# Performance work log

Hardware: AMD Instinct MI355X
Metric: run time of the kernel (lower is better)

Reference implementation:

```python
import jax, jax.numpy as jnp
import numpy as np

B, SQ, SK = 2, 2048, 2048
D, H = 1024, 16
HD = D // H              # head_dim = 64
R = 128                  # rel_pos_max_distance
P = 2 * R + 1            # num_pos_ids = 257
RADIUS = 256             # local_attention_radius


def setup_inputs() -> dict:
    key = jax.random.key(0)
    ks = jax.random.split(key, 8)
    s = 0.02
    return {
        "Q": jax.random.normal(ks[0], (B, SQ, D), dtype=jnp.float32),
        "K": jax.random.normal(ks[1], (B, SK, D), dtype=jnp.float32),
        "V": jax.random.normal(ks[2], (B, SK, D), dtype=jnp.float32),
        "Wq": jax.random.normal(ks[3], (D, D), dtype=jnp.float32) * s,
        "Wk": jax.random.normal(ks[4], (D, D), dtype=jnp.float32) * s,
        "Wv": jax.random.normal(ks[5], (D, D), dtype=jnp.float32) * s,
        "Wo": jax.random.normal(ks[6], (D, D), dtype=jnp.float32) * s,
        "E": jax.random.normal(ks[7], (P, D), dtype=jnp.float32) * s,  # rel_embeds
    }


def _split_heads(x, W):
    # bias-free projection then split: B x S x D -> B x H x S x HD
    y = x @ W.T
    b, s, _ = y.shape
    return y.reshape(b, s, H, HD).transpose(0, 2, 1, 3)


def reference(Q, K, V, Wq, Wk, Wv, Wo, E):
    q = _split_heads(Q, Wq)  # B,H,Sq,HD
    k = _split_heads(K, Wk)  # B,H,Sk,HD
    v = _split_heads(V, Wv)  # B,H,Sk,HD

    # rel_embeds reshape matches torch: E[p] viewed as (head_dim, num_heads)
    rel = E.reshape(P, HD, H).transpose(2, 0, 1)           # H,P,HD
    Q_rel = jnp.einsum("bhqd,hpd->bhqp", q, rel)           # B,H,Sq,P

    # slided relative position ids: clip(j - i, -R, R) + R
    i = jnp.arange(SQ)[:, None]
    j = jnp.arange(SK)[None, :]
    rel_ids = jnp.clip(j - i, -R, R) + R                   # Sq,Sk
    rel_shift = jnp.take_along_axis(
        Q_rel, jnp.broadcast_to(rel_ids, (B, H, SQ, SK)), axis=3
    )                                                       # B,H,Sq,Sk

    energy = (jnp.einsum("bhqd,bhkd->bhqk", q, k) + rel_shift) / jnp.sqrt(
        jnp.float32(HD)
    )

    # local attention mask: True = masked (outside window of radius RADIUS)
    mask = jnp.abs(j - i) > RADIUS                          # Sq,Sk
    mask = mask & ~jnp.all(mask, axis=-1, keepdims=True)    # never mask full rows
    energy = jnp.where(mask[None, None], -jnp.inf, energy)

    attn = jax.nn.softmax(energy, axis=-1)                  # B,H,Sq,Sk
    out = jnp.einsum("bhqk,bhkd->bhqd", attn, v)            # B,H,Sq,HD
    # torch: view(B,H,Sq,HD).permute(0,2,3,1).flatten(2,3) -> B,Sq,(HD*H)
    out = out.transpose(0, 2, 3, 1).reshape(B, SQ, D)
    return out @ Wo.T
```

## Files before the change

### kernel.cpp

```cpp
#include <hip/hip_runtime.h>
#include <hip/hip_bf16.h>

#define BATCH 2
#define SQn 2048
#define SKn 2048
#define DMODEL 1024
#define NH 16
#define HD 64
#define NPOS 257
#define RWIN 128
#define RADIUS 256

typedef __attribute__((ext_vector_type(8))) short bf16x8;
typedef __attribute__((ext_vector_type(4))) float f32x4;

static __device__ __forceinline__ unsigned short f2bf(float f) {
    union { float f; unsigned u; } v; v.f = f;
    unsigned r = (v.u + 0x7FFFu + ((v.u >> 16) & 1u)) >> 16;
    return (unsigned short)r;
}
static __device__ __forceinline__ float bf2f(unsigned short b) {
    union { unsigned u; float f; } v; v.u = ((unsigned)b) << 16;
    return v.f;
}

static __device__ __forceinline__ void gl_lds16(const unsigned short* g, unsigned short* l) {
    __builtin_amdgcn_global_load_lds(
        (const __attribute__((address_space(1))) unsigned*)g,
        (__attribute__((address_space(3))) unsigned*)l, 16, 0, 0);
}

#define SWZ(row) (((row) ^ ((row) >> 2)) & 3)

__global__ __launch_bounds__(256) void convert_kernel(
    const float* __restrict__ Q, const float* __restrict__ K, const float* __restrict__ V,
    const float* __restrict__ Wq, const float* __restrict__ Wk, const float* __restrict__ Wv,
    const float* __restrict__ Wo,
    unsigned short* __restrict__ xb,
    unsigned short* __restrict__ wb,
    unsigned short* __restrict__ woh)
{
    int i = blockIdx.x * 256 + threadIdx.x;
    if (i < 3145728) {
        int which = i >> 20;
        int off = i & 1048575;
        const float* src = which == 0 ? Q : (which == 1 ? K : V);
        unsigned short* dst = xb + (size_t)which * 4194304;
        float4 v4 = ((const float4*)src)[off];
        ushort4 o4;
        o4.x = f2bf(v4.x); o4.y = f2bf(v4.y); o4.z = f2bf(v4.z); o4.w = f2bf(v4.w);
        ((ushort4*)dst)[off] = o4;
    } else {
        int i2 = i - 3145728;
        int which = i2 >> 18;
        int off = i2 & 262143;
        if (which < 3) {
            const float* src = which == 0 ? Wq : (which == 1 ? Wk : Wv);
            unsigned short* dst = wb + (size_t)which * 1048576;
            float4 v4 = ((const float4*)src)[off];
            ushort4 o4;
            o4.x = f2bf(v4.x); o4.y = f2bf(v4.y); o4.z = f2bf(v4.z); o4.w = f2bf(v4.w);
            ((ushort4*)dst)[off] = o4;
        } else {
            float4 v4 = ((const float4*)Wo)[off];
            int e0 = off * 4;
            int n  = e0 >> 10;
            int c0 = e0 & 1023;
            int d  = c0 >> 4;
            int h0 = c0 & 15;
            woh[((size_t)(h0 + 0) * 1024 + n) * 64 + d] = f2bf(v4.x);
            woh[((size_t)(h0 + 1) * 1024 + n) * 64 + d] = f2bf(v4.y);
            woh[((size_t)(h0 + 2) * 1024 + n) * 64 + d] = f2bf(v4.z);
            woh[((size_t)(h0 + 3) * 1024 + n) * 64 + d] = f2bf(v4.w);
        }
    }
}

__global__ __launch_bounds__(256) void mfma_gemm(
    const unsigned short* __restrict__ Xall,
    const unsigned short* __restrict__ Wall,
    unsigned short* __restrict__ Yall)
{
    __shared__ unsigned short sA[128 * 32];
    __shared__ unsigned short sB[128 * 32];
    __shared__ unsigned short sT[64 * 136];

    const int tid  = threadIdx.x;
    const int wv   = tid >> 6;
    const int lane = tid & 63;
    const int quad = lane >> 4;
    const int l15  = lane & 15;
    const int z    = blockIdx.z;
    const int m0   = blockIdx.x * 128;
    const int n0   = blockIdx.y * 128;
    const int wr   = (wv >> 1) * 64;
    const int wc   = (wv & 1) * 64;

    const unsigned short* X = Xall + (size_t)z * (4096 * 1024);
    const unsigned short* W = Wall + (size_t)z * (1024 * 1024);

    int aoff[4], boff[4];
#pragma unroll
    for (int t = 0; t < 4; ++t) {
        int row = wr + t * 16 + l15;
        aoff[t] = row * 32 + ((quad ^ SWZ(row)) * 8);
        int col = wc + t * 16 + l15;
        boff[t] = col * 32 + ((quad ^ SWZ(col)) * 8);
    }

    int srow[2], scg[2], sf[2];
#pragma unroll
    for (int r = 0; r < 2; ++r) {
        int f = r * 256 + tid;
        sf[r] = f;
        srow[r] = f >> 2;
        scg[r] = (f & 3) ^ SWZ(srow[r]);
    }

    f32x4 acc[4][4];
#pragma unroll
    for (int i = 0; i < 4; ++i)
#pragma unroll
        for (int j = 0; j < 4; ++j)
            acc[i][j] = (f32x4){0.f, 0.f, 0.f, 0.f};

    for (int k0 = 0; k0 < 1024; k0 += 32) {
        __syncthreads();
#pragma unroll
        for (int r = 0; r < 2; ++r) {
            gl_lds16(X + (size_t)(m0 + srow[r]) * 1024 + k0 + scg[r] * 8, &sA[sf[r] * 8]);
            gl_lds16(W + (size_t)(n0 + srow[r]) * 1024 + k0 + scg[r] * 8, &sB[sf[r] * 8]);
        }
        __syncthreads();

        bf16x8 af[4], bfr[4];
#pragma unroll
        for (int t = 0; t < 4; ++t) af[t]  = *(const bf16x8*)&sA[aoff[t]];
#pragma unroll
        for (int t = 0; t < 4; ++t) bfr[t] = *(const bf16x8*)&sB[boff[t]];
#pragma unroll
        for (int i = 0; i < 4; ++i)
#pragma unroll
            for (int j = 0; j < 4; ++j)
                acc[i][j] = __builtin_amdgcn_mfma_f32_16x16x32_bf16(af[i], bfr[j], acc[i][j], 0, 0, 0);
    }

    unsigned short* Y = Yall + (size_t)z * (4096 * 1024);
    const int b_ = m0 >> 11;
    const int s0 = m0 & (SQn - 1);

    if (z < 2) {
#pragma unroll
        for (int i = 0; i < 4; ++i) {
            int mbase = s0 + wr + i * 16 + quad * 4;
#pragma unroll
            for (int j = 0; j < 4; ++j) {
                int col = n0 + wc + j * 16 + l15;
                int h = col >> 6, dd = col & 63;
                unsigned short* yb = Y + (((size_t)(b_ * NH + h) * SQn) << 6) + dd;
#pragma unroll
                for (int r = 0; r < 4; ++r)
                    yb[(size_t)(mbase + r) << 6] = f2bf(acc[i][j][r]);
            }
        }
    } else {
#pragma unroll
        for (int hh = 0; hh < 2; ++hh) {
            __syncthreads();
            if ((wv & 1) == hh) {
#pragma unroll
                for (int i = 0; i < 4; ++i) {
                    int mloc = wr + i * 16 + quad * 4;
#pragma unroll
                    for (int j = 0; j < 4; ++j) {
                        ushort4 pk;
                        pk.x = f2bf(acc[i][j][0]);
                        pk.y = f2bf(acc[i][j][1]);
                        pk.z = f2bf(acc[i][j][2]);
                        pk.w = f2bf(acc[i][j][3]);
                        *(ushort4*)&sT[(j * 16 + l15) * 136 + mloc] = pk;
                    }
                }
            }
            __syncthreads();
            int h = (n0 >> 6) + hh;
            unsigned short* yb = Y + ((size_t)(b_ * NH + h) * HD) * SKn + s0;
#pragma unroll
            for (int it = 0; it < 4; ++it) {
                int u = it * 256 + tid;
                int dd = u >> 4, mc = u & 15;
                uint4 val = *(const uint4*)&sT[dd * 136 + mc * 8];
                *(uint4*)(yb + (size_t)dd * SKn + mc * 8) = val;
            }
        }
    }
}

__global__ __launch_bounds__(256) void gemm_out(
    const unsigned short* __restrict__ aoh,
    const unsigned short* __restrict__ woh,
    float* __restrict__ Y)
{
    __shared__ unsigned short sA[64 * 32];
    __shared__ unsigned short sB[128 * 32];

    const int tid  = threadIdx.x;
    const int wv   = tid >> 6;
    const int lane = tid & 63;
    const int quad = lane >> 4;
    const int l15  = lane & 15;
    const int m0   = blockIdx.x * 64;
    const int n0   = blockIdx.y * 128;
    const int wr   = (wv >> 1) * 32;
    const int wc   = (wv & 1) * 64;
    const int b_   = m0 >> 11;
    const int s0   = m0 & (SQn - 1);

    int aoff[2], boff[4];
#pragma unroll
    for (int i = 0; i < 2; ++i) {
        int row = wr + i * 16 + l15;
        aoff[i] = row * 32 + ((quad ^ SWZ(row)) * 8);
    }
#pragma unroll
    for (int j = 0; j < 4; ++j) {
        int col = wc + j * 16 + l15;
        boff[j] = col * 32 + ((quad ^ SWZ(col)) * 8);
    }

    const int arow = tid >> 2;
    const int acs  = (tid & 3) ^ SWZ(arow);
    int bf_[2], brow[2], bcs[2];
#pragma unroll
    for (int r = 0; r < 2; ++r) {
        int f = r * 256 + tid;
        bf_[r] = f; brow[r] = f >> 2; bcs[r] = (f & 3) ^ SWZ(brow[r]);
    }

    f32x4 acc[2][4];
#pragma unroll
    for (int i = 0; i < 2; ++i)
#pragma unroll
        for (int j = 0; j < 4; ++j)
            acc[i][j] = (f32x4){0.f, 0.f, 0.f, 0.f};

    for (int h = 0; h < NH; ++h) {
        const unsigned short* Ah = aoh + ((size_t)(b_ * NH + h) * SQn + s0) * HD;
        const unsigned short* Bh = woh + ((size_t)h * 1024 + n0) * HD;
#pragma unroll
        for (int k0 = 0; k0 < 64; k0 += 32) {
            __syncthreads();
            gl_lds16(Ah + (size_t)arow * HD + k0 + acs * 8, &sA[tid * 8]);
#pragma unroll
            for (int r = 0; r < 2; ++r)
                gl_lds16(Bh + (size_t)brow[r] * HD + k0 + bcs[r] * 8, &sB[bf_[r] * 8]);
            __syncthreads();

            bf16x8 af[2], bfr[4];
#pragma unroll
            for (int i = 0; i < 2; ++i) af[i]  = *(const bf16x8*)&sA[aoff[i]];
#pragma unroll
            for (int j = 0; j < 4; ++j) bfr[j] = *(const bf16x8*)&sB[boff[j]];
#pragma unroll
            for (int i = 0; i < 2; ++i)
#pragma unroll
                for (int j = 0; j < 4; ++j)
                    acc[i][j] = __builtin_amdgcn_mfma_f32_16x16x32_bf16(af[i], bfr[j], acc[i][j], 0, 0, 0);
        }
    }

#pragma unroll
    for (int i = 0; i < 2; ++i) {
        int mbase = m0 + wr + i * 16 + quad * 4;
#pragma unroll
        for (int j = 0; j < 4; ++j) {
            int col = n0 + wc + j * 16 + l15;
#pragma unroll
            for (int r = 0; r < 4; ++r)
                Y[(size_t)(mbase + r) * DMODEL + col] = acc[i][j][r];
        }
    }
}

__global__ __launch_bounds__(256) void relt_kernel(
    const float* __restrict__ E, unsigned short* __restrict__ relTb)
{
    int idx = blockIdx.x * 256 + threadIdx.x;
    const int total = NH * NPOS * HD;
    if (idx < total) {
        int d = idx & (HD - 1);
        int p = (idx >> 6) % NPOS;
        int h = idx / (NPOS * HD);
        relTb[idx] = f2bf(E[(size_t)p * DMODEL + d * NH + h]);
    }
}

#define BIAS_S 9.765625e-4f

__global__ __launch_bounds__(256) void attn_mfma(
    const unsigned short* __restrict__ q,
    const unsigned short* __restrict__ k,
    const unsigned short* __restrict__ vT,
    const unsigned short* __restrict__ relTb,
    unsigned short* __restrict__ aoh)
{
    __shared__ unsigned short sQ[64 * 64];
    __shared__ unsigned short sK[64 * 64];
    __shared__ unsigned short sVt[64 * 64];
    __shared__ unsigned short sP[4][16 * 72];
    __shared__ signed char    sq8[64 * 260];

    const int tid  = threadIdx.x;
    const int w    = tid >> 6;
    const int lane = tid & 63;
    const int quad = lane >> 4;
    const int l15  = lane & 15;
    const int xcd  = blockIdx.x & 7;
    const int sidx = blockIdx.x >> 3;
    const int bh   = (xcd << 2) | (sidx >> 5);
    const int q0   = (sidx & 31) << 6;
    const int h    = bh & (NH - 1);

    const int f1 = tid,       row1 = f1 >> 3;
    const int c1 = ((f1 & 7) ^ (row1 & 7)) * 8;
    const int f2 = 256 + tid, row2 = f2 >> 3;
    const int c2 = ((f2 & 7) ^ (row2 & 7)) * 8;

    {
        const unsigned short* gq = q + ((size_t)bh * SQn + q0) * HD;
        gl_lds16(gq + row1 * HD + c1, &sQ[f1 * 8]);
        gl_lds16(gq + row2 * HD + c2, &sQ[f2 * 8]);
    }
    __syncthreads();

    const int qrow = w * 16 + l15;
    const int qs = (quad ^ (qrow & 7)) * 8;
    bf16x8 a0 = *(const bf16x8*)&sQ[qrow * 64 + qs];
    bf16x8 a1 = *(const bf16x8*)&sQ[qrow * 64 + (qs ^ 32)];

    const int myrow = w * 16 + quad * 4;
    for (int c5 = 0; c5 < 5; ++c5) {
        __syncthreads();
        const unsigned short* gr = relTb + ((size_t)h * NPOS + c5 * 64) * HD;
        gl_lds16(gr + row1 * HD + c1, &sK[f1 * 8]);
        gl_lds16(gr + row2 * HD + c2, &sK[f2 * 8]);
        __syncthreads();
#pragma unroll
        for (int t = 0; t < 4; ++t) {
            int prow = t * 16 + l15;
            int ks = (quad ^ (prow & 7)) * 8;
            bf16x8 b0 = *(const bf16x8*)&sK[prow * 64 + ks];
            bf16x8 b1 = *(const bf16x8*)&sK[prow * 64 + (ks ^ 32)];
            f32x4 cc = {0.f, 0.f, 0.f, 0.f};
            cc = __builtin_amdgcn_mfma_f32_16x16x32_bf16(a0, b0, cc, 0, 0, 0);
            cc = __builtin_amdgcn_mfma_f32_16x16x32_bf16(a1, b1, cc, 0, 0, 0);
            int pos = c5 * 64 + t * 16 + l15;
            if (pos < NPOS) {
#pragma unroll
                for (int r = 0; r < 4; ++r) {
                    int iq = (int)rintf(cc[r] * 128.0f);
                    iq = iq < -127 ? -127 : (iq > 127 ? 127 : iq);
                    sq8[(myrow + r) * 260 + pos] = (signed char)iq;
                }
            }
        }
    }
    __syncthreads();

    float bias0[4], bias256[4];
#pragma unroll
    for (int r = 0; r < 4; ++r) {
        bias0[r]   = (float)sq8[(myrow + r) * 260 + 0]   * BIAS_S;
        bias256[r] = (float)sq8[(myrow + r) * 260 + 256] * BIAS_S;
    }

    const int lo = (q0 - RADIUS) > 0 ? (q0 - RADIUS) : 0;
    const int hi = (q0 + 63 + RADIUS) < (SKn - 1) ? (q0 + 63 + RADIUS) : (SKn - 1);
    const int nt = ((hi - lo) >> 6) + 1;
    const int e_ = l15 - quad * 4;

    const unsigned short* kg = k  + (size_t)bh * SKn * HD;
    const unsigned short* vg = vT + (size_t)bh * HD * SKn;

    float lacc[4] = {0.f, 0.f, 0.f, 0.f};
    f32x4 o[4];
#pragma unroll
    for (int t = 0; t < 4; ++t) o[t] = (f32x4){0.f, 0.f, 0.f, 0.f};

    {
        gl_lds16(kg + (size_t)(lo + row1) * HD + c1, &sK[f1 * 8]);
        gl_lds16(kg + (size_t)(lo + row2) * HD + c2, &sK[f2 * 8]);
        gl_lds16(vg + (size_t)row1 * SKn + lo + c1, &sVt[f1 * 8]);
        gl_lds16(vg + (size_t)row2 * SKn + lo + c2, &sVt[f2 * 8]);
    }

    for (int kt = 0; kt < nt; ++kt) {
        const int kb = lo + (kt << 6);
        __syncthreads();

        bf16x8 kf0[4], kf1[4], vf0[4], vf1[4];
#pragma unroll
        for (int t = 0; t < 4; ++t) {
            int prow = t * 16 + l15;
            int ks = (quad ^ (prow & 7)) * 8;
            kf0[t] = *(const bf16x8*)&sK[prow * 64 + ks];
            kf1[t] = *(const bf16x8*)&sK[prow * 64 + (ks ^ 32)];
            vf0[t] = *(const bf16x8*)&sVt[prow * 64 + ks];
            vf1[t] = *(const bf16x8*)&sVt[prow * 64 + (ks ^ 32)];
        }
        __syncthreads();

        if (kt + 1 < nt) {
            const int kb2 = kb + 64;
            gl_lds16(kg + (size_t)(kb2 + row1) * HD + c1, &sK[f1 * 8]);
            gl_lds16(kg + (size_t)(kb2 + row2) * HD + c2, &sK[f2 * 8]);
            gl_lds16(vg + (size_t)row1 * SKn + kb2 + c1, &sVt[f1 * 8]);
            gl_lds16(vg + (size_t)row2 * SKn + kb2 + c2, &sVt[f2 * 8]);
        }

        const int dtbase = kb - q0 - w * 16;
#pragma unroll
        for (int t = 0; t < 4; ++t) {
            const int dt = dtbase + t * 16;
            const int spb = (quad * 4) * 72 + t * 16 + l15;
            if (dt <= -272 || dt >= 272) {
#pragma unroll
                for (int r = 0; r < 4; ++r) sP[w][spb + r * 72] = 0;
            } else {
                f32x4 sc = {0.f, 0.f, 0.f, 0.f};
                sc = __builtin_amdgcn_mfma_f32_16x16x32_bf16(a0, kf0[t], sc, 0, 0, 0);
                sc = __builtin_amdgcn_mfma_f32_16x16x32_bf16(a1, kf1[t], sc, 0, 0, 0);

                float pv[4];
                if (dt >= -112 && dt <= 112) {
                    int idx0 = myrow * 260 + dt + 128 + e_;
#pragma unroll
                    for (int r = 0; r < 4; ++r) {
                        float bf = (float)sq8[idx0 + r * 259] * BIAS_S;
                        pv[r] = __expf(fmaf(sc[r], 0.125f, bf));
                    }
                } else if (dt >= -240 && dt <= -144) {
#pragma unroll
                    for (int r = 0; r < 4; ++r)
                        pv[r] = __expf(fmaf(sc[r], 0.125f, bias0[r]));
                } else if (dt >= 144 && dt <= 240) {
#pragma unroll
                    for (int r = 0; r < 4; ++r)
                        pv[r] = __expf(fmaf(sc[r], 0.125f, bias256[r]));
                } else {
#pragma unroll
                    for (int r = 0; r < 4; ++r) {
                        int d = dt + e_ - r;
                        bool in = (unsigned)(d + RADIUS) <= 2u * RADIUS;
                        int p = d < -RWIN ? 0 : (d > RWIN ? 2 * RWIN : d + RWIN);
                        float bf = (float)sq8[(myrow + r) * 260 + p] * BIAS_S;
                        float e = __expf(fmaf(sc[r], 0.125f, bf));
                        pv[r] = in ? e : 0.0f;
                    }
                }
#pragma unroll
                for (int r = 0; r < 4; ++r) {
                    unsigned short pb = f2bf(pv[r]);
                    sP[w][spb + r * 72] = pb;
                    lacc[r] += bf2f(pb);
                }
            }
        }

        bf16x8 p0 = *(const bf16x8*)&sP[w][l15 * 72 + quad * 8];
        bf16x8 p1 = *(const bf16x8*)&sP[w][l15 * 72 + 32 + quad * 8];
#pragma unroll
        for (int t = 0; t < 4; ++t) {
            o[t] = __builtin_amdgcn_mfma_f32_16x16x32_bf16(p0, vf0[t], o[t], 0, 0, 0);
            o[t] = __builtin_amdgcn_mfma_f32_16x16x32_bf16(p1, vf1[t], o[t], 0, 0, 0);
        }
    }

    float linv[4];
#pragma unroll
    for (int r = 0; r < 4; ++r) {
        float l = lacc[r];
#pragma unroll
        for (int off = 1; off <= 8; off <<= 1) l += __shfl_xor(l, off);
        linv[r] = 1.0f / l;
    }

    unsigned short* ob = aoh + ((size_t)bh * SQn + q0) * HD;
#pragma unroll
    for (int t = 0; t < 4; ++t) {
#pragma unroll
        for (int r = 0; r < 4; ++r) {
            int irow = w * 16 + quad * 4 + r;
            ob[irow * HD + t * 16 + l15] = f2bf(o[t][r] * linv[r]);
        }
    }
}

extern "C" void kernel_launch(void* const* d_in, const int* in_sizes, int n_in,
                              void* d_out, int out_size, void* d_ws, size_t ws_size,
                              hipStream_t stream) {
    const float* Q  = (const float*)d_in[0];
    const float* K  = (const float*)d_in[1];
    const float* V  = (const float*)d_in[2];
    const float* Wq = (const float*)d_in[3];
    const float* Wk = (const float*)d_in[4];
    const float* Wv = (const float*)d_in[5];
    const float* Wo = (const float*)d_in[6];
    const float* E  = (const float*)d_in[7];
    float* out = (float*)d_out;

    char* p = (char*)d_ws;
    unsigned short* xb    = (unsigned short*)p; p += (size_t)24 << 20;
    unsigned short* wb    = (unsigned short*)p; p += (size_t)6  << 20;
    unsigned short* woh   = (unsigned short*)p; p += (size_t)2  << 20;
    unsigned short* head  = (unsigned short*)p; p += (size_t)24 << 20;
    unsigned short* relTb = (unsigned short*)p; p += (size_t)1  << 20;
    unsigned short* aoh   = (unsigned short*)p;

    unsigned short* qb  = head;
    unsigned short* kb  = head + 4194304;
    unsigned short* vTb = head + 8388608;

    dim3 bb(256);
    convert_kernel<<<dim3(16384), bb, 0, stream>>>(Q, K, V, Wq, Wk, Wv, Wo, xb, wb, woh);
    relt_kernel<<<dim3(1028), bb, 0, stream>>>(E, relTb);
    mfma_gemm<<<dim3(32, 8, 3), bb, 0, stream>>>(xb, wb, head);
    attn_mfma<<<dim3(BATCH * NH * (SQn / 64)), bb, 0, stream>>>(qb, kb, vTb, relTb, aoh);
    gemm_out<<<dim3(64, 8), bb, 0, stream>>>(aoh, woh, out);
}
```

Baseline: 212.4 us.

## Double-buffer output GEMM, widen attention blocks to 128 queries, use exp2

The output projection GEMM now loads a full 64-wide head slice per stage and double-buffers it in shared memory, so it needs one barrier per head instead of two per half-head. The attention kernel moves to 512-thread blocks covering 128 query rows, letting each K/V tile load serve twice as many queries. It reuses the int8 bias buffer as the Q staging area, skips whole tiles that fall outside a wave's window, and folds log2(e) into the scales so it can call exp2 directly. It also raises wave priority around the PV MFMAs. The larger blocks use more shared memory and registers per block, which may reduce occupancy.

```diff
diff --git a/kernel.cpp b/kernel.cpp
--- a/kernel.cpp
+++ b/kernel.cpp
@@ -201,8 +201,7 @@
     const unsigned short* __restrict__ woh,
     float* __restrict__ Y)
 {
-    __shared__ unsigned short sA[64 * 32];
-    __shared__ unsigned short sB[128 * 32];
+    __shared__ unsigned short S[24576];
 
     const int tid  = threadIdx.x;
     const int wv   = tid >> 6;
@@ -216,25 +215,34 @@
     const int b_   = m0 >> 11;
     const int s0   = m0 & (SQn - 1);
 
-    int aoff[2], boff[4];
-#pragma unroll
-    for (int i = 0; i < 2; ++i) {
-        int row = wr + i * 16 + l15;
-        aoff[i] = row * 32 + ((quad ^ SWZ(row)) * 8);
-    }
-#pragma unroll
-    for (int j = 0; j < 4; ++j) {
-        int col = wc + j * 16 + l15;
-        boff[j] = col * 32 + ((quad ^ SWZ(col)) * 8);
-    }
-
-    const int arow = tid >> 2;
-    const int acs  = (tid & 3) ^ SWZ(arow);
-    int bf_[2], brow[2], bcs[2];
-#pragma unroll
-    for (int r = 0; r < 2; ++r) {
-        int f = r * 256 + tid;
-        bf_[r] = f; brow[r] = f >> 2; bcs[r] = (f & 3) ^ SWZ(brow[r]);
+    int rowa[2], ca[2];
+#pragma unroll
+    for (int it = 0; it < 2; ++it) {
+        int f = it * 256 + tid;
+        rowa[it] = f >> 3;
+        ca[it]   = ((f & 7) ^ (rowa[it] & 7)) * 8;
+    }
+    int rowb[4], cb[4];
+#pragma unroll
+    for (int it = 0; it < 4; ++it) {
+        int f = it * 256 + tid;
+        rowb[it] = f >> 3;
+        cb[it]   = ((f & 7) ^ (rowb[it] & 7)) * 8;
+    }
+
+    int aoff[2][2], boff[2][4];
+#pragma unroll
+    for (int ks = 0; ks < 2; ++ks) {
+#pragma unroll
+        for (int i = 0; i < 2; ++i) {
+            int R = wr + i * 16 + l15;
+            aoff[ks][i] = R * 64 + ((((ks << 2) + quad) ^ (R & 7)) * 8);
+        }
+#pragma unroll
+        for (int j = 0; j < 4; ++j) {
+            int C = wc + j * 16 + l15;
+            boff[ks][j] = C * 64 + ((((ks << 2) + quad) ^ (C & 7)) * 8);
+        }
     }
 
     f32x4 acc[2][4];
@@ -244,29 +252,59 @@
         for (int j = 0; j < 4; ++j)
             acc[i][j] = (f32x4){0.f, 0.f, 0.f, 0.f};
 
+    {
+        const unsigned short* Ah = aoh + ((size_t)(b_ * NH) * SQn + s0) * HD;
+        const unsigned short* Bh = woh + (size_t)n0 * HD;
+#pragma unroll
+        for (int it = 0; it < 2; ++it)
+            gl_lds16(Ah + (size_t)rowa[it] * HD + ca[it], &S[(it * 256 + tid) * 8]);
+#pragma unroll
+        for (int it = 0; it < 4; ++it)
+            gl_lds16(Bh + (size_t)rowb[it] * HD + cb[it], &S[8192 + (it * 256 + tid) * 8]);
+    }
+
     for (int h = 0; h < NH; ++h) {
-        const unsigned short* Ah = aoh + ((size_t)(b_ * NH + h) * SQn + s0) * HD;
-        const unsigned short* Bh = woh + ((size_t)h * 1024 + n0) * HD;
-#pragma unroll
-        for (int k0 = 0; k0 < 64; k0 += 32) {
-            __syncthreads();
-            gl_lds16(Ah + (size_t)arow * HD + k0 + acs * 8, &sA[tid * 8]);
-#pragma unroll
-            for (int r = 0; r < 2; ++r)
-                gl_lds16(Bh + (size_t)brow[r] * HD + k0 + bcs[r] * 8, &sB[bf_[r] * 8]);
-            __syncthreads();
-
-            bf16x8 af[2], bfr[4];
-#pragma unroll
-            for (int i = 0; i < 2; ++i) af[i]  = *(const bf16x8*)&sA[aoff[i]];
-#pragma unroll
-            for (int j = 0; j < 4; ++j) bfr[j] = *(const bf16x8*)&sB[boff[j]];
-#pragma unroll
-            for (int i = 0; i < 2; ++i)
-#pragma unroll
-                for (int j = 0; j < 4; ++j)
-                    acc[i][j] = __builtin_amdgcn_mfma_f32_16x16x32_bf16(af[i], bfr[j], acc[i][j], 0, 0, 0);
-        }
+        const int cur = h & 1;
+        __syncthreads();
+
+        if (h + 1 < NH) {
+            const int nxt = cur ^ 1;
+            const unsigned short* Ah = aoh + ((size_t)(b_ * NH + h + 1) * SQn + s0) * HD;
+            const unsigned short* Bh = woh + ((size_t)(h + 1) * 1024 + n0) * HD;
+#pragma unroll
+            for (int it = 0; it < 2; ++it)
+                gl_lds16(Ah + (size_t)rowa[it] * HD + ca[it],
+                         &S[nxt * 4096 + (it * 256 + tid) * 8]);
+#pragma unroll
+            for (int it = 0; it < 4; ++it)
+                gl_lds16(Bh + (size_t)rowb[it] * HD + cb[it],
+                         &S[8192 + nxt * 8192 + (it * 256 + tid) * 8]);
+        }
+
+        const unsigned short* bA = &S[cur * 4096];
+        const unsigned short* bB = &S[8192 + cur * 8192];
+
+        bf16x8 a0[2], b0[4];
+#pragma unroll
+        for (int i = 0; i < 2; ++i) a0[i] = *(const bf16x8*)&bA[aoff[0][i]];
+#pragma unroll
+        for (int j = 0; j < 4; ++j) b0[j] = *(const bf16x8*)&bB[boff[0][j]];
+#pragma unroll
+        for (int i = 0; i < 2; ++i)
+#pragma unroll
+            for (int j = 0; j < 4; ++j)
+                acc[i][j] = __builtin_amdgcn_mfma_f32_16x16x32_bf16(a0[i], b0[j], acc[i][j], 0, 0, 0);
+
+        bf16x8 a1[2], b1[4];
+#pragma unroll
+        for (int i = 0; i < 2; ++i) a1[i] = *(const bf16x8*)&bA[aoff[1][i]];
+#pragma unroll
+        for (int j = 0; j < 4; ++j) b1[j] = *(const bf16x8*)&bB[boff[1][j]];
+#pragma unroll
+        for (int i = 0; i < 2; ++i)
+#pragma unroll
+            for (int j = 0; j < 4; ++j)
+                acc[i][j] = __builtin_amdgcn_mfma_f32_16x16x32_bf16(a1[i], b1[j], acc[i][j], 0, 0, 0);
     }
 
 #pragma unroll
@@ -295,20 +333,21 @@
     }
 }
 
-#define BIAS_S 9.765625e-4f
-
-__global__ __launch_bounds__(256) void attn_mfma(
+#define BIAS_S2 0.0014089565402528222f
+#define SC2     0.1803368801111204f
+
+__global__ __launch_bounds__(512, 4) void attn_mfma(
     const unsigned short* __restrict__ q,
     const unsigned short* __restrict__ k,
     const unsigned short* __restrict__ vT,
     const unsigned short* __restrict__ relTb,
     unsigned short* __restrict__ aoh)
 {
-    __shared__ unsigned short sQ[64 * 64];
     __shared__ unsigned short sK[64 * 64];
     __shared__ unsigned short sVt[64 * 64];
-    __shared__ unsigned short sP[4][16 * 72];
-    __shared__ signed char    sq8[64 * 260];
+    __shared__ unsigned short sP[8][16 * 72];
+    __shared__ signed char    sq8[128 * 260];
+    unsigned short* const sQ = (unsigned short*)sq8;
 
     const int tid  = threadIdx.x;
     const int w    = tid >> 6;
@@ -317,19 +356,22 @@
     const int l15  = lane & 15;
     const int xcd  = blockIdx.x & 7;
     const int sidx = blockIdx.x >> 3;
-    const int bh   = (xcd << 2) | (sidx >> 5);
-    const int q0   = (sidx & 31) << 6;
+    const int bh   = (xcd << 2) | (sidx >> 4);
+    const int q0   = (sidx & 15) << 7;
     const int h    = bh & (NH - 1);
 
-    const int f1 = tid,       row1 = f1 >> 3;
-    const int c1 = ((f1 & 7) ^ (row1 & 7)) * 8;
-    const int f2 = 256 + tid, row2 = f2 >> 3;
-    const int c2 = ((f2 & 7) ^ (row2 & 7)) * 8;
+    const int row1 = tid >> 3;
+    const int c1   = ((tid & 7) ^ (row1 & 7)) * 8;
 
     {
         const unsigned short* gq = q + ((size_t)bh * SQn + q0) * HD;
-        gl_lds16(gq + row1 * HD + c1, &sQ[f1 * 8]);
-        gl_lds16(gq + row2 * HD + c2, &sQ[f2 * 8]);
+#pragma unroll
+        for (int it = 0; it < 2; ++it) {
+            int f = it * 512 + tid;
+            int row = f >> 3;
+            int c = ((f & 7) ^ (row & 7)) * 8;
+            gl_lds16(gq + row * HD + c, &sQ[f * 8]);
+        }
     }
     __syncthreads();
 
@@ -342,8 +384,7 @@
     for (int c5 = 0; c5 < 5; ++c5) {
         __syncthreads();
         const unsigned short* gr = relTb + ((size_t)h * NPOS + c5 * 64) * HD;
-        gl_lds16(gr + row1 * HD + c1, &sK[f1 * 8]);
-        gl_lds16(gr + row2 * HD + c2, &sK[f2 * 8]);
+        gl_lds16(gr + row1 * HD + c1, &sK[tid * 8]);
         __syncthreads();
 #pragma unroll
         for (int t = 0; t < 4; ++t) {
@@ -370,12 +411,12 @@
     float bias0[4], bias256[4];
 #pragma unroll
     for (int r = 0; r < 4; ++r) {
-        bias0[r]   = (float)sq8[(myrow + r) * 260 + 0]   * BIAS_S;
-        bias256[r] = (float)sq8[(myrow + r) * 260 + 256] * BIAS_S;
+        bias0[r]   = (float)sq8[(myrow + r) * 260 + 0]   * BIAS_S2;
+        bias256[r] = (float)sq8[(myrow + r) * 260 + 256] * BIAS_S2;
     }
 
     const int lo = (q0 - RADIUS) > 0 ? (q0 - RADIUS) : 0;
-    const int hi = (q0 + 63 + RADIUS) < (SKn - 1) ? (q0 + 63 + RADIUS) : (SKn - 1);
+    const int hi = (q0 + 127 + RADIUS) < (SKn - 1) ? (q0 + 127 + RADIUS) : (SKn - 1);
     const int nt = ((hi - lo) >> 6) + 1;
     const int e_ = l15 - quad * 4;
 
@@ -388,10 +429,8 @@
     for (int t = 0; t < 4; ++t) o[t] = (f32x4){0.f, 0.f, 0.f, 0.f};
 
     {
-        gl_lds16(kg + (size_t)(lo + row1) * HD + c1, &sK[f1 * 8]);
-        gl_lds16(kg + (size_t)(lo + row2) * HD + c2, &sK[f2 * 8]);
-        gl_lds16(vg + (size_t)row1 * SKn + lo + c1, &sVt[f1 * 8]);
-        gl_lds16(vg + (size_t)row2 * SKn + lo + c2, &sVt[f2 * 8]);
+        gl_lds16(kg + (size_t)(lo + row1) * HD + c1, &sK[tid * 8]);
+        gl_lds16(vg + (size_t)row1 * SKn + lo + c1, &sVt[tid * 8]);
     }
 
     for (int kt = 0; kt < nt; ++kt) {
@@ -412,67 +451,68 @@
 
         if (kt + 1 < nt) {
             const int kb2 = kb + 64;
-            gl_lds16(kg + (size_t)(kb2 + row1) * HD + c1, &sK[f1 * 8]);
-            gl_lds16(kg + (size_t)(kb2 + row2) * HD + c2, &sK[f2 * 8]);
-            gl_lds16(vg + (size_t)row1 * SKn + kb2 + c1, &sVt[f1 * 8]);
-            gl_lds16(vg + (size_t)row2 * SKn + kb2 + c2, &sVt[f2 * 8]);
+            gl_lds16(kg + (size_t)(kb2 + row1) * HD + c1, &sK[tid * 8]);
+            gl_lds16(vg + (size_t)row1 * SKn + kb2 + c1, &sVt[tid * 8]);
         }
 
         const int dtbase = kb - q0 - w * 16;
-#pragma unroll
-        for (int t = 0; t < 4; ++t) {
-            const int dt = dtbase + t * 16;
-            const int spb = (quad * 4) * 72 + t * 16 + l15;
-            if (dt <= -272 || dt >= 272) {
-#pragma unroll
-                for (int r = 0; r < 4; ++r) sP[w][spb + r * 72] = 0;
-            } else {
-                f32x4 sc = {0.f, 0.f, 0.f, 0.f};
-                sc = __builtin_amdgcn_mfma_f32_16x16x32_bf16(a0, kf0[t], sc, 0, 0, 0);
-                sc = __builtin_amdgcn_mfma_f32_16x16x32_bf16(a1, kf1[t], sc, 0, 0, 0);
-
-                float pv[4];
-                if (dt >= -112 && dt <= 112) {
-                    int idx0 = myrow * 260 + dt + 128 + e_;
+        if (dtbase > -320 && dtbase < 272) {
+#pragma unroll
+            for (int t = 0; t < 4; ++t) {
+                const int dt = dtbase + t * 16;
+                const int spb = (quad * 4) * 72 + t * 16 + l15;
+                if (dt <= -272 || dt >= 272) {
+#pragma unroll
+                    for (int r = 0; r < 4; ++r) sP[w][spb + r * 72] = 0;
+                } else {
+                    f32x4 sc = {0.f, 0.f, 0.f, 0.f};
+                    sc = __builtin_amdgcn_mfma_f32_16x16x32_bf16(a0, kf0[t], sc, 0, 0, 0);
+                    sc = __builtin_amdgcn_mfma_f32_16x16x32_bf16(a1, kf1[t], sc, 0, 0, 0);
+
+                    float pv[4];
+                    if (dt >= -112 && dt <= 112) {
+                        int idx0 = myrow * 260 + dt + 128 + e_;
+#pragma unroll
+                        for (int r = 0; r < 4; ++r) {
+                            float bf = (float)sq8[idx0 + r * 259] * BIAS_S2;
+                            pv[r] = __builtin_amdgcn_exp2f(fmaf(sc[r], SC2, bf));
+                        }
+                    } else if (dt >= -240 && dt <= -144) {
+#pragma unroll
+                        for (int r = 0; r < 4; ++r)
+                            pv[r] = __builtin_amdgcn_exp2f(fmaf(sc[r], SC2, bias0[r]));
+                    } else if (dt >= 144 && dt <= 240) {
+#pragma unroll
+                        for (int r = 0; r < 4; ++r)
+                            pv[r] = __builtin_amdgcn_exp2f(fmaf(sc[r], SC2, bias256[r]));
+                    } else {
+#pragma unroll
+                        for (int r = 0; r < 4; ++r) {
+                            int d = dt + e_ - r;
+                            bool in = (unsigned)(d + RADIUS) <= 2u * RADIUS;
+                            int p = d < -RWIN ? 0 : (d > RWIN ? 2 * RWIN : d + RWIN);
+                            float bf = (float)sq8[(myrow + r) * 260 + p] * BIAS_S2;
+                            float e = __builtin_amdgcn_exp2f(fmaf(sc[r], SC2, bf));
+                            pv[r] = in ? e : 0.0f;
+                        }
+                    }
 #pragma unroll
                     for (int r = 0; r < 4; ++r) {
-                        float bf = (float)sq8[idx0 + r * 259] * BIAS_S;
-                        pv[r] = __expf(fmaf(sc[r], 0.125f, bf));
-                    }
-                } else if (dt >= -240 && dt <= -144) {
-#pragma unroll
-                    for (int r = 0; r < 4; ++r)
-                        pv[r] = __expf(fmaf(sc[r], 0.125f, bias0[r]));
-                } else if (dt >= 144 && dt <= 240) {
-#pragma unroll
-                    for (int r = 0; r < 4; ++r)
-                        pv[r] = __expf(fmaf(sc[r], 0.125f, bias256[r]));
-                } else {
-#pragma unroll
-                    for (int r = 0; r < 4; ++r) {
-                        int d = dt + e_ - r;
-                        bool in = (unsigned)(d + RADIUS) <= 2u * RADIUS;
-                        int p = d < -RWIN ? 0 : (d > RWIN ? 2 * RWIN : d + RWIN);
-                        float bf = (float)sq8[(myrow + r) * 260 + p] * BIAS_S;
-                        float e = __expf(fmaf(sc[r], 0.125f, bf));
-                        pv[r] = in ? e : 0.0f;
+                        unsigned short pb = f2bf(pv[r]);
+                        sP[w][spb + r * 72] = pb;
+                        lacc[r] += bf2f(pb);
                     }
                 }
-#pragma unroll
-                for (int r = 0; r < 4; ++r) {
-                    unsigned short pb = f2bf(pv[r]);
-                    sP[w][spb + r * 72] = pb;
-                    lacc[r] += bf2f(pb);
-                }
             }
-        }
-
-        bf16x8 p0 = *(const bf16x8*)&sP[w][l15 * 72 + quad * 8];
-        bf16x8 p1 = *(const bf16x8*)&sP[w][l15 * 72 + 32 + quad * 8];
-#pragma unroll
-        for (int t = 0; t < 4; ++t) {
-            o[t] = __builtin_amdgcn_mfma_f32_16x16x32_bf16(p0, vf0[t], o[t], 0, 0, 0);
-            o[t] = __builtin_amdgcn_mfma_f32_16x16x32_bf16(p1, vf1[t], o[t], 0, 0, 0);
+            bf16x8 p0 = *(const bf16x8*)&sP[w][l15 * 72 + quad * 8];
+            bf16x8 p1 = *(const bf16x8*)&sP[w][l15 * 72 + 32 + quad * 8];
+            __builtin_amdgcn_s_setprio(1);
+#pragma unroll
+            for (int t = 0; t < 4; ++t) {
+                o[t] = __builtin_amdgcn_mfma_f32_16x16x32_bf16(p0, vf0[t], o[t], 0, 0, 0);
+                o[t] = __builtin_amdgcn_mfma_f32_16x16x32_bf16(p1, vf1[t], o[t], 0, 0, 0);
+            }
+            __builtin_amdgcn_s_setprio(0);
         }
     }
 
@@ -525,6 +565,6 @@
     convert_kernel<<<dim3(16384), bb, 0, stream>>>(Q, K, V, Wq, Wk, Wv, Wo, xb, wb, woh);
     relt_kernel<<<dim3(1028), bb, 0, stream>>>(E, relTb);
     mfma_gemm<<<dim3(32, 8, 3), bb, 0, stream>>>(xb, wb, head);
-    attn_mfma<<<dim3(BATCH * NH * (SQn / 64)), bb, 0, stream>>>(qb, kb, vTb, relTb, aoh);
+    attn_mfma<<<dim3(BATCH * NH * (SQn / 128)), dim3(512), 0, stream>>>(qb, kb, vTb, relTb, aoh);
     gemm_out<<<dim3(64, 8), bb, 0, stream>>>(aoh, woh, out);
 }
```

New measurement: 197.0 us. -7.2%, faster.
